# Performance work log

Measured on AMD Instinct MI355X. Metric: run time of the kernel, lower is better.

## Reference

```python
import jax, jax.numpy as jnp
import numpy as np
from jax import lax

V, E, H, B, LP, LQ = 50000, 300, 150, 32, 400, 50


def setup_inputs() -> dict:
    key = jax.random.key(0)
    ks = iter(jax.random.split(key, 40))

    def nrm(shape, s=0.05):
        return jax.random.normal(next(ks), shape, jnp.float32) * s

    emb = nrm((V, E)).at[0].set(0.0)  # padding_idx=0 row is zero
    return dict(
        passage_ids=jax.random.randint(next(ks), (LP, B), 1, V, jnp.int32),
        question_ids=jax.random.randint(next(ks), (LQ, B), 1, V, jnp.int32),
        passage_lens=jax.random.randint(next(ks), (B,), LP // 2, LP + 1, jnp.int32),
        question_lens=jax.random.randint(next(ks), (B,), LQ // 2, LQ + 1, jnp.int32),
        emb=emb,
        plstm_Wih=nrm((4 * H, E)), plstm_Whh=nrm((4 * H, H)), plstm_b=nrm((4 * H,)),
        Wq=nrm((H, H)), Wp=nrm((H, H)), bp=nrm((H,)), Wr=nrm((H, H)),
        wa=nrm((H,)), ba=nrm(()),
        mf_Wih=nrm((4 * H, 2 * H)), mf_Whh=nrm((4 * H, H)), mf_b=nrm((4 * H,)),
        mb_Wih=nrm((4 * H, 2 * H)), mb_Whh=nrm((4 * H, H)), mb_b=nrm((4 * H,)),
        Vm=nrm((H, 2 * H)), Wa_ans=nrm((H, H)), ba_ans=nrm((H,)),
        wb=nrm((H,)), bb=nrm(()),
        ap_Wih=nrm((4 * H, 2 * H)), ap_Whh=nrm((4 * H, H)), ap_b=nrm((4 * H,)),
    )


def _cell(x, h, c, Wih, Whh, b):
    # torch LSTMCell: gate order i, f, g, o; b = b_ih + b_hh
    g = x @ Wih.T + h @ Whh.T + b
    i, f, gg, o = jnp.split(g, 4, axis=-1)
    c2 = jax.nn.sigmoid(f) * c + jax.nn.sigmoid(i) * jnp.tanh(gg)
    return jax.nn.sigmoid(o) * jnp.tanh(c2), c2


def _run_lstm(x, Wih, Whh, b):
    z = jnp.zeros((x.shape[1], Whh.shape[1]), x.dtype)

    def step(carry, xt):
        h, c = carry
        h2, c2 = _cell(xt, h, c, Wih, Whh, b)
        return (h2, c2), h2

    return lax.scan(step, (z, z), x)[1]


def reference(passage_ids, question_ids, passage_lens, question_lens, emb,
              plstm_Wih, plstm_Whh, plstm_b, Wq, Wp, bp, Wr, wa, ba,
              mf_Wih, mf_Whh, mf_b, mb_Wih, mb_Whh, mb_b,
              Vm, Wa_ans, ba_ans, wb, bb, ap_Wih, ap_Whh, ap_b):
    p_mask = (jnp.arange(LP)[:, None] < passage_lens[None, :]).astype(jnp.float32)  # [LP,B]
    q_mask = (jnp.arange(LQ)[:, None] < question_lens[None, :]).astype(jnp.float32)  # [LQ,B]
    # NB: original code (bug) encodes BOTH passage and question with passage_lstm
    Hp = _run_lstm(emb[passage_ids], plstm_Wih, plstm_Whh, plstm_b) * p_mask[:, :, None]
    Hq = _run_lstm(emb[question_ids], plstm_Wih, plstm_Whh, plstm_b) * q_mask[:, :, None]
    aq = Hq @ Wq.T  # [LQ,B,H]

    def match(Hp_seq, m_seq, Wih, Whh, b):
        z0 = jnp.zeros((B, H), jnp.float32)

        def step(carry, inputs):
            h, c = carry
            hp_t, m_t = inputs  # [B,H], [B]
            g = jnp.tanh(aq + (hp_t @ Wp.T + bp)[None] + (h @ Wr.T)[None])  # [LQ,B,H]
            alpha = jax.nn.softmax(g @ wa + ba, axis=0)  # softmax over question positions, [LQ,B]
            wq_t = jnp.einsum('lb,lbh->bh', alpha, Hq)
            zt = jnp.concatenate([hp_t, wq_t], axis=-1) * m_t[:, None]
            h2, c2 = _cell(zt, h, c, Wih, Whh, b)
            h2 = h2 * m_t[:, None]
            c2 = c2 * m_t[:, None]
            return (h2, c2), h2

        return lax.scan(step, (z0, z0), (Hp_seq, m_seq))[1]

    Hf = match(Hp, p_mask, mf_Wih, mf_Whh, mf_b)                    # [LP,B,H]
    Hb = match(Hp[::-1], p_mask[::-1], mb_Wih, mb_Whh, mb_b)[::-1]  # [LP,B,H]
    Hr = jnp.concatenate([Hf, Hb], axis=-1)  # [LP,B,2H]
    am = Hr @ Vm.T  # [LP,B,H]

    ha = jnp.zeros((B, H), jnp.float32)
    ca = jnp.zeros((B, H), jnp.float32)
    dists = []
    for _ in range(2):  # answer-pointer: start / end
        Fk = jnp.tanh(am + (ha @ Wa_ans.T + ba_ans)[None])
        beta = jax.nn.softmax(Fk @ wb + bb, axis=0)  # [LP,B]
        dists.append(beta)
        wHr = jnp.einsum('lb,lbh->bh', beta, Hr)
        ha, ca = _cell(wHr, ha, ca, ap_Wih, ap_Whh, ap_b)
    return jnp.stack(dists)  # [2, LP, B]
```

## Files before the change

### kernel.cpp

```cpp
#include <hip/hip_runtime.h>


typedef _Float16 f16;
typedef f16 f16x2 __attribute__((ext_vector_type(2)));
typedef unsigned int u32;
typedef unsigned short u16;

constexpr int cLP = 400, cLQ = 50, cB = 32, cH = 150, cG = 600;

__device__ __forceinline__ float exp2_(float x){
#if __has_builtin(__builtin_amdgcn_exp2f)
  return __builtin_amdgcn_exp2f(x);
#else
  return exp2f(x);
#endif
}
__device__ __forceinline__ float rcp_(float x){
#if __has_builtin(__builtin_amdgcn_rcpf)
  return __builtin_amdgcn_rcpf(x);
#else
  return 1.0f / x;
#endif
}
__device__ __forceinline__ float sigm(float x){ return rcp_(1.f + exp2_(-1.44269504f * x)); }
__device__ __forceinline__ float tanh_(float x){ return 1.f - 2.f * rcp_(1.f + exp2_(2.88539008f * x)); }

union U2 { u32 u; f16x2 h; };

__device__ __forceinline__ float fdot2_(u32 a, u32 b, float c){
  U2 ua, ub; ua.u = a; ub.u = b;
#if __has_builtin(__builtin_amdgcn_fdot2)
  return __builtin_amdgcn_fdot2(ua.h, ub.h, c, false);
#else
  return c + (float)ua.h[0] * (float)ub.h[0] + (float)ua.h[1] * (float)ub.h[1];
#endif
}
__device__ __forceinline__ u32 pack2(float x, float y){
  U2 p; p.h[0] = (f16)x; p.h[1] = (f16)y; return p.u;
}
__device__ __forceinline__ float2 unp2(u32 v){
  U2 p; p.u = v; return make_float2((float)p.h[0], (float)p.h[1]);
}

__device__ __forceinline__ uint4 ldw4(const float* __restrict__ wr, int i){
  uint4 r;
  r.x = pack2(wr[8*i+0], wr[8*i+1]);
  r.y = pack2(wr[8*i+2], wr[8*i+3]);
  r.z = pack2(wr[8*i+4], wr[8*i+5]);
  r.w = pack2(wr[8*i+6], wr[8*i+7]);
  return r;
}

#define PIN4(v) asm volatile("" : "+v"(v.x), "+v"(v.y), "+v"(v.z), "+v"(v.w));
#define PIN4W(i) PIN4(w##i)
#define PIN4Q(i) PIN4(q##i)

#define REP10(M) M(0) M(1) M(2) M(3) M(4) M(5) M(6) M(7) M(8) M(9)
#define REP6(M) M(0) M(1) M(2) M(3) M(4) M(5)

__global__ __launch_bounds__(256)
void gemm_k(const float* __restrict__ A, const int* __restrict__ ids,
            const float* __restrict__ emb,
            const float* __restrict__ W, int ldw, const float* __restrict__ bias,
            float* __restrict__ Cf, f16* __restrict__ Ch,
            int M, int N, int K)
{
  __shared__ __align__(16) float As[16][68];
  __shared__ __align__(16) float Wt[16][68];
  __shared__ int sids[64];
  int tid = threadIdx.x;
  int n0 = blockIdx.x * 64;
  int m0 = blockIdx.y * 64;
  int tx = tid & 15, ty = tid >> 4;
  if (ids){ if (tid < 64) sids[tid] = ids[m0 + tid]; }
  __syncthreads();

  float acc[4][4] = {};
  int sm = tid >> 2;
  int kq = (tid & 3) << 2;
  const float* arow = ids ? (emb + (size_t)sids[sm] * K)
                          : (A   + (size_t)(m0 + sm) * K);
  const float* wrow = W + (size_t)(n0 + sm) * ldw;
  bool nok = (n0 + sm) < N;

  for (int k0 = 0; k0 < K; k0 += 16){
    #pragma unroll
    for (int p = 0; p < 4; p++){
      int kk = kq + p, k = k0 + kk;
      As[kk][sm] = (k < K) ? arow[k] : 0.f;
      Wt[kk][sm] = (nok && k < K) ? wrow[k] : 0.f;
    }
    __syncthreads();
    #pragma unroll
    for (int kk = 0; kk < 16; kk++){
      float4 av = *(const float4*)&As[kk][ty << 2];
      float4 wv = *(const float4*)&Wt[kk][tx << 2];
      float a[4] = {av.x, av.y, av.z, av.w};
      float w[4] = {wv.x, wv.y, wv.z, wv.w};
      #pragma unroll
      for (int i = 0; i < 4; i++)
        #pragma unroll
        for (int j = 0; j < 4; j++)
          acc[i][j] += a[i] * w[j];
    }
    __syncthreads();
  }
  float bj[4];
  #pragma unroll
  for (int j = 0; j < 4; j++){
    int n = n0 + (tx << 2) + j;
    bj[j] = (bias && n < N) ? bias[n] : 0.f;
  }
  #pragma unroll
  for (int i = 0; i < 4; i++){
    int m = m0 + (ty << 2) + i;
    #pragma unroll
    for (int j = 0; j < 4; j++){
      int n = n0 + (tx << 2) + j;
      if (n < N){
        size_t ci = (size_t)m * N + n;
        float v = acc[i][j] + bj[j];
        if (Ch) Ch[ci] = (f16)v; else Cf[ci] = v;
      }
    }
  }
}

__attribute__((amdgpu_waves_per_eu(1, 3)))
__global__ __launch_bounds__(640)
void enc_k(const float* __restrict__ XGp, const float* __restrict__ XGq,
           const float* __restrict__ Whh,
           const int* __restrict__ plens, const int* __restrict__ qlens,
           float* __restrict__ Hp, float* __restrict__ Hq)
{
  int wg = blockIdx.x;
  bool isq = wg >= cB;
  int b = wg & (cB - 1);
  const float* XG = isq ? XGq : XGp;
  float* Hout = isq ? Hq : Hp;
  int T   = isq ? cLQ : cLP;
  int len = (isq ? qlens : plens)[b];
  int tid = threadIdx.x;

  __shared__ __align__(16) u32 WhhL4[9 * 600 * 4];
  __shared__ float c[cH], gl[cG];
  __shared__ __align__(16) u32 h2s[80];

#define DECLW(i) uint4 w##i;
  REP10(DECLW)
#undef DECLW
  {
    const float* wr = Whh + (size_t)(tid < cG ? tid : 0) * cH;
#define LOADW(i) w##i = ldw4(wr, i);
    REP10(LOADW)
#undef LOADW
    REP10(PIN4W)
  }
  for (int idx = tid; idx < 9 * 600; idx += 640){
    int p4 = idx / 600, r = idx % 600;
    const float* wrow = Whh + (size_t)r * cH + 80;
    uint4 v;
    if (p4 < 8) v = ldw4(wrow, p4);
    else {
      v.x = pack2(wrow[64], wrow[65]);
      v.y = pack2(wrow[66], wrow[67]);
      v.z = pack2(wrow[68], wrow[69]);
      v.w = 0;
    }
    *(uint4*)&WhhL4[idx * 4] = v;
  }
  if (tid < cH) c[tid] = 0.f;
  if (tid < 80) h2s[tid] = 0;
  __syncthreads();

  float xgCur = 0.f;
  if (tid < cG) xgCur = XG[(size_t)b * cG + tid];

  for (int t = 0; t < T; t++){
    int tn = (t + 1 < T) ? t + 1 : t;
    float xgN = 0.f;
    if (tid < cG) xgN = XG[((size_t)tn * cB + b) * cG + tid];

    if (tid < cG){
      float aA = 0.f, aB = 0.f, aC = 0.f, aD = 0.f;
#define DOTW(i) { uint4 hq = *(const uint4*)&h2s[4*(i)]; \
      aA = fdot2_(hq.x, w##i.x, aA); aB = fdot2_(hq.y, w##i.y, aB); \
      aC = fdot2_(hq.z, w##i.z, aC); aD = fdot2_(hq.w, w##i.w, aD); }
      REP10(DOTW)
#undef DOTW
      #pragma unroll
      for (int p4 = 0; p4 < 9; p4++){
        uint4 hq = *(const uint4*)&h2s[40 + 4 * p4];
        uint4 wv = *(const uint4*)&WhhL4[(p4 * 600 + tid) * 4];
        aA = fdot2_(hq.x, wv.x, aA);
        aB = fdot2_(hq.y, wv.y, aB);
        aC = fdot2_(hq.z, wv.z, aC);
        aD = fdot2_(hq.w, wv.w, aD);
      }
      gl[tid] = xgCur + ((aA + aB) + (aC + aD));
    }
    __syncthreads();
    if (tid < 75){
      float hv[2];
      #pragma unroll
      for (int z = 0; z < 2; z++){
        int u = 2 * tid + z;
        float ig = sigm(gl[u]);
        float fg = sigm(gl[cH + u]);
        float gg = tanh_(gl[2 * cH + u]);
        float og = sigm(gl[3 * cH + u]);
        float c2 = fg * c[u] + ig * gg;
        float hh = og * tanh_(c2);
        c[u] = c2;
        hv[z] = hh;
      }
      h2s[tid] = pack2(hv[0], hv[1]);
      float mk = (t < len) ? 1.f : 0.f;
      float2 st; st.x = hv[0] * mk; st.y = hv[1] * mk;
      *(float2*)&Hout[((size_t)t * cB + b) * cH + 2 * tid] = st;
    }
    __syncthreads();
    xgCur = xgN;
  }
}

__attribute__((amdgpu_waves_per_eu(1, 3)))
__global__ __launch_bounds__(640)
void match_k(const f16* __restrict__ XAf, const f16* __restrict__ XAb,
             const f16* __restrict__ QWf, const f16* __restrict__ QWb,
             const float* __restrict__ aq, const float* __restrict__ pp,
             const float* __restrict__ mfWhh, const float* __restrict__ mbWhh,
             const float* __restrict__ mfb, const float* __restrict__ mbb,
             const float* __restrict__ Wr, const float* __restrict__ wa,
             const int* __restrict__ plens, float* __restrict__ Hr)
{
  constexpr int NPAD = 160;
  int wg = blockIdx.x;
  int dir = wg >> 5;
  int b = wg & 31;
  const f16* XA = dir ? XAb : XAf;
  const f16* QW = dir ? QWb : QWf;
  const float* Whh = dir ? mbWhh : mfWhh;
  const float* bm  = dir ? mbb   : mfb;
  int len = plens[b];
  int tid = threadIdx.x;

  __shared__ __align__(16) u32 WhhL4[9 * 600 * 4];
  __shared__ __align__(16) u32 WrT4[20 * 150 * 4];
  __shared__ __align__(16) u32 aq3[cLQ * 96];
  __shared__ float gl[cG];
  __shared__ __align__(16) float sc[NPAD];
  __shared__ __align__(16) float waS[NPAD];
  __shared__ float c[cH];
  __shared__ __align__(16) f16 hsf[160];
  __shared__ float loge[64];
  __shared__ __align__(16) u32 alpha2[28];

#define DECLW(i) uint4 w##i;
  REP10(DECLW)
#undef DECLW
  float bk = 0.f;
  {
    const float* wr = Whh + (size_t)(tid < cG ? tid : 0) * cH;
#define LOADW(i) w##i = ldw4(wr, i);
    REP10(LOADW)
#undef LOADW
    REP10(PIN4W)
    if (tid < cG) bk = bm[tid];
  }
#define DECLQ(i) uint4 q##i;
  REP6(DECLQ)
#undef DECLQ
  u32 q24s;
  {
    const u16* QWu = (const u16*)QW;
    int row = (tid < cG) ? tid : 0;
#define QP(p) ((u32)QWu[((size_t)(2*(p)) * cB + b) * cG + row] | \
               ((u32)QWu[((size_t)(2*(p)+1) * cB + b) * cG + row] << 16))
#define LOADQ(i) q##i.x = QP(4*(i)+0); q##i.y = QP(4*(i)+1); \
                 q##i.z = QP(4*(i)+2); q##i.w = QP(4*(i)+3);
    LOADQ(0) LOADQ(1) LOADQ(2) LOADQ(3) LOADQ(4) LOADQ(5)
    q24s = QP(24);
#undef LOADQ
#undef QP
    REP6(PIN4Q)
    asm volatile("" : "+v"(q24s));
  }
  for (int idx = tid; idx < 9 * 600; idx += 640){
    int p4 = idx / 600, r = idx % 600;
    const float* wrow = Whh + (size_t)r * cH + 80;
    uint4 v;
    if (p4 < 8) v = ldw4(wrow, p4);
    else {
      v.x = pack2(wrow[64], wrow[65]);
      v.y = pack2(wrow[66], wrow[67]);
      v.z = pack2(wrow[68], wrow[69]);
      v.w = 0;
    }
    *(uint4*)&WhhL4[idx * 4] = v;
  }
  for (int idx = tid; idx < 20 * 150; idx += 640){
    int i = idx / 150, j = idx % 150;
    const float* wrow = Wr + (size_t)j * cH;
    uint4 v = {0, 0, 0, 0};
    if (i < 18) v = ldw4(wrow, i);
    else if (i == 18){
      v.x = pack2(wrow[144], wrow[145]);
      v.y = pack2(wrow[146], wrow[147]);
      v.z = pack2(wrow[148], wrow[149]);
      v.w = 0;
    }
    *(uint4*)&WrT4[idx * 4] = v;
  }
  for (int idx = tid; idx < cLQ * 96; idx += 640){
    int l = idx / 96, s = idx % 96;
    int ch = s / 12, t = s % 12;
    u32 v = 0;
    if (t < 10){
      int p = ch * 10 + t;
      if (p < 75){
        const float* ap = aq + ((size_t)l * cB + b) * cH;
        v = pack2(ap[2 * p], ap[2 * p + 1]);
      }
    }
    aq3[idx] = v;
  }
  for (int i = tid; i < NPAD; i += 640) waS[i] = (i < cH) ? wa[i] : 0.f;
  if (tid < cH) c[tid] = 0.f;
  if (tid < 160) hsf[tid] = (f16)0.f;
  if (tid >= cH && tid < NPAD) sc[tid] = 0.f;
  if (tid >= 25 && tid < 28) alpha2[tid] = 0;
  __syncthreads();

  f16 xaCurH = (f16)0.f, xaNxtH = (f16)0.f;
  float ppCur = 0.f, ppNxt = 0.f;
  {
    int t0 = dir ? (cLP - 1) : 0;
    if (tid < cG) xaCurH = XA[((size_t)t0 * cB + b) * cG + tid];
    if (tid < cG && (tid & 3) == 0)
      ppCur = pp[((size_t)t0 * cB + b) * cH + (tid >> 2)];
  }

  for (int s = 0; s < cLP; s++){
    int tt = dir ? (cLP - 1 - s) : s;
    float mk = (tt < len) ? 1.f : 0.f;

    {
      int sn = (s + 1 < cLP) ? s + 1 : s;
      int tn = dir ? (cLP - 1 - sn) : sn;
      if (tid < cG) xaNxtH = XA[((size_t)tn * cB + b) * cG + tid];
      if (tid < cG && (tid & 3) == 0)
        ppNxt = pp[((size_t)tn * cB + b) * cH + (tid >> 2)];
    }

    if (tid < cG){
      int q = tid & 3, j = tid >> 2;
      float sA = 0.f, sB = 0.f, sC = 0.f, sD = 0.f;
      #pragma unroll
      for (int i0 = 0; i0 < 5; i0++){
        int i = 5 * q + i0;
        uint4 hq = *(const uint4*)&hsf[8 * i];
        uint4 wv = *(const uint4*)&WrT4[(i * 150 + j) * 4];
        sA = fdot2_(hq.x, wv.x, sA);
        sB = fdot2_(hq.y, wv.y, sB);
        sC = fdot2_(hq.z, wv.z, sC);
        sD = fdot2_(hq.w, wv.w, sD);
      }
      float v = (sA + sB) + (sC + sD);
      v += __shfl_xor(v, 1);
      v += __shfl_xor(v, 2);
      if (q == 0) sc[j] = v + ppCur;
    }
    __syncthreads();

    if (tid < cG){
      float aA = 0.f, aB = 0.f, aC = 0.f, aD = 0.f;
#define DOTW(i) { uint4 hq = *(const uint4*)&hsf[8*(i)]; \
      aA = fdot2_(hq.x, w##i.x, aA); aB = fdot2_(hq.y, w##i.y, aB); \
      aC = fdot2_(hq.z, w##i.z, aC); aD = fdot2_(hq.w, w##i.w, aD); }
      REP10(DOTW)
#undef DOTW
      #pragma unroll
      for (int p4 = 0; p4 < 9; p4++){
        uint4 hq = *(const uint4*)&hsf[80 + 8 * p4];
        uint4 wv = *(const uint4*)&WhhL4[(p4 * 600 + tid) * 4];
        aA = fdot2_(hq.x, wv.x, aA);
        aB = fdot2_(hq.y, wv.y, aB);
        aC = fdot2_(hq.z, wv.z, aC);
        aD = fdot2_(hq.w, wv.w, aD);
      }
      gl[tid] = bk + ((aA + aB) + (aC + aD));
    }
    if (tid < 400){
      int l = tid >> 3, q8 = tid & 7;
      const u32* ab = aq3 + l * 96 + q8 * 12;
      uint4 A0 = *(const uint4*)(ab);
      uint4 A1 = *(const uint4*)(ab + 4);
      uint2 A2 = *(const uint2*)(ab + 8);
      u32 aqp[10] = {A0.x, A0.y, A0.z, A0.w, A1.x, A1.y, A1.z, A1.w, A2.x, A2.y};
      const float4* scv = (const float4*)(sc  + 20 * q8);
      const float4* wav = (const float4*)(waS + 20 * q8);
      float p0 = 0.f, p1 = 0.f;
      #pragma unroll
      for (int i = 0; i < 5; i++){
        float4 sv = scv[i];
        float4 wv = wav[i];
        float2 a0 = unp2(aqp[2 * i]);
        float2 a1 = unp2(aqp[2 * i + 1]);
        p0 += wv.x * rcp_(1.f + exp2_(2.88539008f * (a0.x + sv.x)));
        p1 += wv.y * rcp_(1.f + exp2_(2.88539008f * (a0.y + sv.y)));
        p0 += wv.z * rcp_(1.f + exp2_(2.88539008f * (a1.x + sv.z)));
        p1 += wv.w * rcp_(1.f + exp2_(2.88539008f * (a1.y + sv.w)));
      }
      float part = p0 + p1;
      part += __shfl_xor(part, 1);
      part += __shfl_xor(part, 2);
      part += __shfl_xor(part, 4);
      if (q8 == 0) loge[l] = part;
    }
    __syncthreads();

    if (tid < 64){
      float lg = (tid < cLQ) ? (-2.f * loge[tid]) : -1e30f;
      float mx = lg;
      #pragma unroll
      for (int off = 32; off; off >>= 1) mx = fmaxf(mx, __shfl_xor(mx, off));
      float e = (tid < cLQ) ? exp2_((lg - mx) * 1.44269504f) : 0.f;
      float sum = e;
      #pragma unroll
      for (int off = 32; off; off >>= 1) sum += __shfl_xor(sum, off);
      float al = e * rcp_(sum);
      float alhi = __shfl_down(al, 1);
      if (tid < cLQ && !(tid & 1)) alpha2[tid >> 1] = pack2(al, alhi);
    }
    __syncthreads();

    if (tid < cG){
      float qA = 0.f, qB = 0.f;
#define DOTQ(i) { uint4 a4 = *(const uint4*)&alpha2[4*(i)]; \
      qA = fdot2_(a4.x, q##i.x, qA); qB = fdot2_(a4.y, q##i.y, qB); \
      qA = fdot2_(a4.z, q##i.z, qA); qB = fdot2_(a4.w, q##i.w, qB); }
      REP6(DOTQ)
#undef DOTQ
      qA = fdot2_(alpha2[24], q24s, qA);
      gl[tid] = gl[tid] + mk * ((float)xaCurH + (qA + qB));
    }
    __syncthreads();

    if (tid < cH){
      float ig = sigm(gl[tid]);
      float fg = sigm(gl[cH + tid]);
      float gg = tanh_(gl[2 * cH + tid]);
      float og = sigm(gl[3 * cH + tid]);
      float c2 = (fg * c[tid] + ig * gg) * mk;
      float hh = og * tanh_(c2) * mk;
      c[tid] = c2;
      hsf[tid] = (f16)hh;
      Hr[((size_t)tt * cB + b) * (2 * cH) + dir * cH + tid] = hh;
    }
    __syncthreads();

    xaCurH = xaNxtH;
    ppCur  = ppNxt;
  }
}

__global__ __launch_bounds__(640)
void ptr_k(const float* __restrict__ am, const float* __restrict__ Hr,
           const float* __restrict__ Wa, const float* __restrict__ baa,
           const float* __restrict__ wb,
           const float* __restrict__ apWih, const float* __restrict__ apWhh,
             const float* __restrict__ apb, float* __restrict__ out)
{
  int b = blockIdx.x, tid = threadIdx.x;
  __shared__ float ha[cH], ca[cH], haWa[160], wbs[160];
  __shared__ float beta[cLP], wHr[2 * cH], gl[cG], red[20];
  if (tid < cH){ ha[tid] = 0.f; ca[tid] = 0.f; }
  if (tid < 160) wbs[tid] = (tid < cH) ? wb[tid] : 0.f;
  __syncthreads();

  for (int it = 0; it < 2; ++it){
    if (tid < cH){
      float acc = baa[tid];
      const float* wr = Wa + (size_t)tid * cH;
      for (int i = 0; i < cH; i++) acc += ha[i] * wr[i];
      haWa[tid] = acc;
    } else if (tid < 160) haWa[tid] = 0.f;
    __syncthreads();

    {
      int tt = tid >> 4;
      int jq = tid & 15;
      for (int t0 = 0; t0 < cLP; t0 += 40){
        int t = t0 + tt;
        float part = 0.f;
        const float* amr = am + ((size_t)t * cB + b) * cH;
        #pragma unroll
        for (int i = 0; i < 10; i++){
          int j = jq * 10 + i;
          if (j < cH){
            float F = tanh_(amr[j] + haWa[j]);
            part += wbs[j] * F;
          }
        }
        part += __shfl_xor(part, 1);
        part += __shfl_xor(part, 2);
        part += __shfl_xor(part, 4);
        part += __shfl_xor(part, 8);
        if (jq == 0) beta[t] = part;
      }
    }
    __syncthreads();

    float x = (tid < cLP) ? beta[tid] : -1e30f;
    float mx = x;
    #pragma unroll
    for (int off = 32; off; off >>= 1) mx = fmaxf(mx, __shfl_xor(mx, off));
    if ((tid & 63) == 0) red[tid >> 6] = mx;
    __syncthreads();
    if (tid == 0){
      float m2 = red[0];
      for (int w = 1; w < 10; w++) m2 = fmaxf(m2, red[w]);
      red[16] = m2;
    }
    __syncthreads();
    mx = red[16];
    float e = (tid < cLP) ? exp2_((x - mx) * 1.44269504f) : 0.f;
    float sm = e;
    #pragma unroll
    for (int off = 32; off; off >>= 1) sm += __shfl_xor(sm, off);
    if ((tid & 63) == 0) red[tid >> 6] = sm;
    __syncthreads();
    if (tid == 0){
      float s2 = 0.f;
      for (int w = 0; w < 10; w++) s2 += red[w];
      red[17] = s2;
    }
    __syncthreads();
    float bsum = red[17];
    if (tid < cLP){
      float bt = e * rcp_(bsum);
      beta[tid] = bt;
      out[(size_t)it * cLP * cB + (size_t)tid * cB + b] = bt;
    }
    __syncthreads();

    if (tid < 2 * cH){
      float acc = 0.f;
      for (int t = 0; t < cLP; t++)
        acc += beta[t] * Hr[((size_t)t * cB + b) * (2 * cH) + tid];
      wHr[tid] = acc;
    }
    __syncthreads();

    if (tid < cG){
      float acc = apb[tid];
      const float* r1 = apWih + (size_t)tid * (2 * cH);
      for (int i = 0; i < 2 * cH; i++) acc += wHr[i] * r1[i];
      const float* r2 = apWhh + (size_t)tid * cH;
      for (int i = 0; i < cH; i++) acc += ha[i] * r2[i];
      gl[tid] = acc;
    }
    __syncthreads();
    if (tid < cH){
      float ig = sigm(gl[tid]);
      float fg = sigm(gl[cH + tid]);
      float gg = tanh_(gl[2 * cH + tid]);
      float og = sigm(gl[3 * cH + tid]);
      float c2 = fg * ca[tid] + ig * gg;
      ca[tid] = c2;
      ha[tid] = og * tanh_(c2);
    }
    __syncthreads();
  }
}

extern "C" void kernel_launch(void* const* d_in, const int* in_sizes, int n_in,
                              void* d_out, int out_size, void* d_ws, size_t ws_size,
                              hipStream_t stream)
{
  (void)in_sizes; (void)n_in; (void)out_size; (void)ws_size;
  const int*   p_ids = (const int*)d_in[0];
  const int*   q_ids = (const int*)d_in[1];
  const int*   plens = (const int*)d_in[2];
  const int*   qlens = (const int*)d_in[3];
  const float* emb   = (const float*)d_in[4];
  const float* pWih  = (const float*)d_in[5];
  const float* pWhh  = (const float*)d_in[6];
  const float* pb    = (const float*)d_in[7];
  const float* Wq    = (const float*)d_in[8];
  const float* Wp    = (const float*)d_in[9];
  const float* bp    = (const float*)d_in[10];
  const float* Wr    = (const float*)d_in[11];
  const float* wa    = (const float*)d_in[12];
  const float* mfWih = (const float*)d_in[14];
  const float* mfWhh = (const float*)d_in[15];
  const float* mfb   = (const float*)d_in[16];
  const float* mbWih = (const float*)d_in[17];
  const float* mbWhh = (const float*)d_in[18];
  const float* mbb   = (const float*)d_in[19];
  const float* Vm    = (const float*)d_in[20];
  const float* Waa   = (const float*)d_in[21];
  const float* baa   = (const float*)d_in[22];
  const float* wb    = (const float*)d_in[23];
  const float* apWih = (const float*)d_in[25];
  const float* apWhh = (const float*)d_in[26];
  const float* apb   = (const float*)d_in[27];
  float* out = (float*)d_out;

  float* ws  = (float*)d_ws;
  float* XGp = ws;
  float* XGq = ws + 7680000;
  f16*   XAb = (f16*)(ws + 8640000);
  float* Hp  = ws + 12480000;
  float* Hq  = ws + 14400000;
  float* aqb = ws + 14640000;
  float* ppb = ws + 14880000;
  float* Hr  = ws + 16800000;
  float* am  = ws + 20640000;
  f16*   XAf = (f16*)XGp;
  f16*   QWf = (f16*)XGq;
  f16*   QWb = QWf + (size_t)1600 * 600;

  dim3 blk(256);
  gemm_k<<<dim3(10,200), blk, 0, stream>>>(nullptr, p_ids, emb, pWih, 300, pb,
                                           XGp, nullptr, 12800, 600, 300);
  gemm_k<<<dim3(10, 25), blk, 0, stream>>>(nullptr, q_ids, emb, pWih, 300, pb,
                                           XGq, nullptr, 1600, 600, 300);
  enc_k<<<64, 640, 0, stream>>>(XGp, XGq, pWhh, plens, qlens, Hp, Hq);
  gemm_k<<<dim3(3,200), blk, 0, stream>>>(Hp, nullptr, nullptr, Wp, 150, bp,
                                          ppb, nullptr, 12800, 150, 150);
  gemm_k<<<dim3(3, 25), blk, 0, stream>>>(Hq, nullptr, nullptr, Wq, 150, nullptr,
                                          aqb, nullptr, 1600, 150, 150);
  gemm_k<<<dim3(10,200), blk, 0, stream>>>(Hp, nullptr, nullptr, mfWih, 300, nullptr,
                                           nullptr, XAf, 12800, 600, 150);
  gemm_k<<<dim3(10,200), blk, 0, stream>>>(Hp, nullptr, nullptr, mbWih, 300, nullptr,
                                           nullptr, XAb, 12800, 600, 150);
  gemm_k<<<dim3(10, 25), blk, 0, stream>>>(Hq, nullptr, nullptr, mfWih + 150, 300, nullptr,
                                           nullptr, QWf, 1600, 600, 150);
  gemm_k<<<dim3(10, 25), blk, 0, stream>>>(Hq, nullptr, nullptr, mbWih + 150, 300, nullptr,
                                           nullptr, QWb, 1600, 600, 150);
  match_k<<<64, 640, 0, stream>>>(XAf, XAb, QWf, QWb, aqb, ppb, mfWhh, mbWhh,
                                  mfb, mbb, Wr, wa, plens, Hr);
  gemm_k<<<dim3(3,200), blk, 0, stream>>>(Hr, nullptr, nullptr, Vm, 300, nullptr,
                                          am, nullptr, 12800, 150, 300);
  ptr_k<<<32, 640, 0, stream>>>(am, Hr, Waa, baa, wb, apWih, apWhh, apb, out);
}
```

Baseline: 2.238 ms.

## Remap gate rows so LSTM cell update uses wave shuffles, removing barriers

Threads are remapped so each 64-lane wave holds all four gates (i,f,g,o) for 16 hidden units, with the gate index in bits 4-5 of the lane id. Gate nonlinearities are then computed in parallel per lane and combined through cross-lane shuffles, which removes the gl shared buffer and one barrier per timestep in both the encoder and match kernels. In the match kernel the Wr score dot product is also merged into the same phase as the Whh dot, dropping another barrier. The cost is 640 threads with some idle lanes (u>=150) and a wider f16 hidden buffer in the encoder.

Result: slower. 4.071 ms (+81.9%).

```diff
diff --git a/kernel.cpp b/kernel.cpp
--- a/kernel.cpp
+++ b/kernel.cpp
@@ -141,24 +141,28 @@
   int T   = isq ? cLQ : cLP;
   int len = (isq ? qlens : plens)[b];
   int tid = threadIdx.x;
+  int u = (tid & 15) + ((tid >> 6) << 4);
+  int q = (tid >> 4) & 3;
+  int r = q * cH + u;
+  bool act = (u < cH);
 
   __shared__ __align__(16) u32 WhhL4[9 * 600 * 4];
-  __shared__ float c[cH], gl[cG];
-  __shared__ __align__(16) u32 h2s[80];
+  __shared__ float c[cH];
+  __shared__ __align__(16) f16 hsf[160];
 
 #define DECLW(i) uint4 w##i;
   REP10(DECLW)
 #undef DECLW
   {
-    const float* wr = Whh + (size_t)(tid < cG ? tid : 0) * cH;
+    const float* wr = Whh + (size_t)(act ? r : 0) * cH;
 #define LOADW(i) w##i = ldw4(wr, i);
     REP10(LOADW)
 #undef LOADW
     REP10(PIN4W)
   }
   for (int idx = tid; idx < 9 * 600; idx += 640){
-    int p4 = idx / 600, r = idx % 600;
-    const float* wrow = Whh + (size_t)r * cH + 80;
+    int p4 = idx / 600, rr = idx % 600;
+    const float* wrow = Whh + (size_t)rr * cH + 80;
     uint4 v;
     if (p4 < 8) v = ldw4(wrow, p4);
     else {
@@ -170,54 +174,46 @@
     *(uint4*)&WhhL4[idx * 4] = v;
   }
   if (tid < cH) c[tid] = 0.f;
-  if (tid < 80) h2s[tid] = 0;
+  if (tid < 160) hsf[tid] = (f16)0.f;
   __syncthreads();
 
   float xgCur = 0.f;
-  if (tid < cG) xgCur = XG[(size_t)b * cG + tid];
+  if (act) xgCur = XG[(size_t)b * cG + r];
 
   for (int t = 0; t < T; t++){
     int tn = (t + 1 < T) ? t + 1 : t;
     float xgN = 0.f;
-    if (tid < cG) xgN = XG[((size_t)tn * cB + b) * cG + tid];
-
-    if (tid < cG){
+    if (act) xgN = XG[((size_t)tn * cB + b) * cG + r];
+
+    if (act){
       float aA = 0.f, aB = 0.f, aC = 0.f, aD = 0.f;
-#define DOTW(i) { uint4 hq = *(const uint4*)&h2s[4*(i)]; \
+#define DOTW(i) { uint4 hq = *(const uint4*)&hsf[8*(i)]; \
       aA = fdot2_(hq.x, w##i.x, aA); aB = fdot2_(hq.y, w##i.y, aB); \
       aC = fdot2_(hq.z, w##i.z, aC); aD = fdot2_(hq.w, w##i.w, aD); }
       REP10(DOTW)
 #undef DOTW
       #pragma unroll
       for (int p4 = 0; p4 < 9; p4++){
-        uint4 hq = *(const uint4*)&h2s[40 + 4 * p4];
-        uint4 wv = *(const uint4*)&WhhL4[(p4 * 600 + tid) * 4];
+        uint4 hq = *(const uint4*)&hsf[80 + 8 * p4];
+        uint4 wv = *(const uint4*)&WhhL4[(p4 * 600 + r) * 4];
         aA = fdot2_(hq.x, wv.x, aA);
         aB = fdot2_(hq.y, wv.y, aB);
         aC = fdot2_(hq.z, wv.z, aC);
         aD = fdot2_(hq.w, wv.w, aD);
       }
-      gl[tid] = xgCur + ((aA + aB) + (aC + aD));
-    }
-    __syncthreads();
-    if (tid < 75){
-      float hv[2];
-      #pragma unroll
-      for (int z = 0; z < 2; z++){
-        int u = 2 * tid + z;
-        float ig = sigm(gl[u]);
-        float fg = sigm(gl[cH + u]);
-        float gg = tanh_(gl[2 * cH + u]);
-        float og = sigm(gl[3 * cH + u]);
-        float c2 = fg * c[u] + ig * gg;
-        float hh = og * tanh_(c2);
+      float gv = xgCur + ((aA + aB) + (aC + aD));
+      float tv = (q == 2) ? tanh_(gv) : sigm(gv);
+      float tB = __shfl_xor(tv, 16);
+      float tC = __shfl_xor(tv, 32);
+      float tD = __shfl_xor(tB, 32);
+      if (q == 0){
+        float c2 = tB * c[u] + tv * tC;
+        float hh = tD * tanh_(c2);
         c[u] = c2;
-        hv[z] = hh;
-      }
-      h2s[tid] = pack2(hv[0], hv[1]);
-      float mk = (t < len) ? 1.f : 0.f;
-      float2 st; st.x = hv[0] * mk; st.y = hv[1] * mk;
-      *(float2*)&Hout[((size_t)t * cB + b) * cH + 2 * tid] = st;
+        hsf[u] = (f16)hh;
+        float mk = (t < len) ? 1.f : 0.f;
+        Hout[((size_t)t * cB + b) * cH + u] = hh * mk;
+      }
     }
     __syncthreads();
     xgCur = xgN;
@@ -244,11 +240,14 @@
   const float* bm  = dir ? mbb   : mfb;
   int len = plens[b];
   int tid = threadIdx.x;
+  int u = (tid & 15) + ((tid >> 6) << 4);
+  int q = (tid >> 4) & 3;
+  int r = q * cH + u;
+  bool act = (u < cH);
 
   __shared__ __align__(16) u32 WhhL4[9 * 600 * 4];
   __shared__ __align__(16) u32 WrT4[20 * 150 * 4];
   __shared__ __align__(16) u32 aq3[cLQ * 96];
-  __shared__ float gl[cG];
   __shared__ __align__(16) float sc[NPAD];
   __shared__ __align__(16) float waS[NPAD];
   __shared__ float c[cH];
@@ -261,12 +260,12 @@
 #undef DECLW
   float bk = 0.f;
   {
-    const float* wr = Whh + (size_t)(tid < cG ? tid : 0) * cH;
+    const float* wr = Whh + (size_t)(act ? r : 0) * cH;
 #define LOADW(i) w##i = ldw4(wr, i);
     REP10(LOADW)
 #undef LOADW
     REP10(PIN4W)
-    if (tid < cG) bk = bm[tid];
+    if (act) bk = bm[r];
   }
 #define DECLQ(i) uint4 q##i;
   REP6(DECLQ)
@@ -274,7 +273,7 @@
   u32 q24s;
   {
     const u16* QWu = (const u16*)QW;
-    int row = (tid < cG) ? tid : 0;
+    int row = act ? r : 0;
 #define QP(p) ((u32)QWu[((size_t)(2*(p)) * cB + b) * cG + row] | \
                ((u32)QWu[((size_t)(2*(p)+1) * cB + b) * cG + row] << 16))
 #define LOADQ(i) q##i.x = QP(4*(i)+0); q##i.y = QP(4*(i)+1); \
@@ -287,8 +286,8 @@
     asm volatile("" : "+v"(q24s));
   }
   for (int idx = tid; idx < 9 * 600; idx += 640){
-    int p4 = idx / 600, r = idx % 600;
-    const float* wrow = Whh + (size_t)r * cH + 80;
+    int p4 = idx / 600, rr = idx % 600;
+    const float* wrow = Whh + (size_t)rr * cH + 80;
     uint4 v;
     if (p4 < 8) v = ldw4(wrow, p4);
     else {
@@ -336,9 +335,8 @@
   float ppCur = 0.f, ppNxt = 0.f;
   {
     int t0 = dir ? (cLP - 1) : 0;
-    if (tid < cG) xaCurH = XA[((size_t)t0 * cB + b) * cG + tid];
-    if (tid < cG && (tid & 3) == 0)
-      ppCur = pp[((size_t)t0 * cB + b) * cH + (tid >> 2)];
+    if (act) xaCurH = XA[((size_t)t0 * cB + b) * cG + r];
+    if (act && q == 0) ppCur = pp[((size_t)t0 * cB + b) * cH + u];
   }
 
   for (int s = 0; s < cLP; s++){
@@ -348,32 +346,12 @@
     {
       int sn = (s + 1 < cLP) ? s + 1 : s;
       int tn = dir ? (cLP - 1 - sn) : sn;
-      if (tid < cG) xaNxtH = XA[((size_t)tn * cB + b) * cG + tid];
-      if (tid < cG && (tid & 3) == 0)
-        ppNxt = pp[((size_t)tn * cB + b) * cH + (tid >> 2)];
-    }
-
-    if (tid < cG){
-      int q = tid & 3, j = tid >> 2;
-      float sA = 0.f, sB = 0.f, sC = 0.f, sD = 0.f;
-      #pragma unroll
-      for (int i0 = 0; i0 < 5; i0++){
-        int i = 5 * q + i0;
-        uint4 hq = *(const uint4*)&hsf[8 * i];
-        uint4 wv = *(const uint4*)&WrT4[(i * 150 + j) * 4];
-        sA = fdot2_(hq.x, wv.x, sA);
-        sB = fdot2_(hq.y, wv.y, sB);
-        sC = fdot2_(hq.z, wv.z, sC);
-        sD = fdot2_(hq.w, wv.w, sD);
-      }
-      float v = (sA + sB) + (sC + sD);
-      v += __shfl_xor(v, 1);
-      v += __shfl_xor(v, 2);
-      if (q == 0) sc[j] = v + ppCur;
-    }
-    __syncthreads();
-
-    if (tid < cG){
+      if (act) xaNxtH = XA[((size_t)tn * cB + b) * cG + r];
+      if (act && q == 0) ppNxt = pp[((size_t)tn * cB + b) * cH + u];
+    }
+
+    float gpre = 0.f;
+    if (act){
       float aA = 0.f, aB = 0.f, aC = 0.f, aD = 0.f;
 #define DOTW(i) { uint4 hq = *(const uint4*)&hsf[8*(i)]; \
       aA = fdot2_(hq.x, w##i.x, aA); aB = fdot2_(hq.y, w##i.y, aB); \
@@ -383,14 +361,32 @@
       #pragma unroll
       for (int p4 = 0; p4 < 9; p4++){
         uint4 hq = *(const uint4*)&hsf[80 + 8 * p4];
-        uint4 wv = *(const uint4*)&WhhL4[(p4 * 600 + tid) * 4];
+        uint4 wv = *(const uint4*)&WhhL4[(p4 * 600 + r) * 4];
         aA = fdot2_(hq.x, wv.x, aA);
         aB = fdot2_(hq.y, wv.y, aB);
         aC = fdot2_(hq.z, wv.z, aC);
         aD = fdot2_(hq.w, wv.w, aD);
       }
-      gl[tid] = bk + ((aA + aB) + (aC + aD));
-    }
+      gpre = bk + ((aA + aB) + (aC + aD));
+
+      float sA = 0.f, sB = 0.f, sC = 0.f, sD = 0.f;
+      #pragma unroll
+      for (int i0 = 0; i0 < 5; i0++){
+        int i = 5 * q + i0;
+        uint4 hq = *(const uint4*)&hsf[8 * i];
+        uint4 wv = *(const uint4*)&WrT4[(i * 150 + u) * 4];
+        sA = fdot2_(hq.x, wv.x, sA);
+        sB = fdot2_(hq.y, wv.y, sB);
+        sC = fdot2_(hq.z, wv.z, sC);
+        sD = fdot2_(hq.w, wv.w, sD);
+      }
+      float v = (sA + sB) + (sC + sD);
+      v += __shfl_xor(v, 16);
+      v += __shfl_xor(v, 32);
+      if (q == 0) sc[u] = v + ppCur;
+    }
+    __syncthreads();
+
     if (tid < 400){
       int l = tid >> 3, q8 = tid & 7;
       const u32* ab = aq3 + l * 96 + q8 * 12;
@@ -435,7 +431,7 @@
     }
     __syncthreads();
 
-    if (tid < cG){
+    if (act){
       float qA = 0.f, qB = 0.f;
 #define DOTQ(i) { uint4 a4 = *(const uint4*)&alpha2[4*(i)]; \
       qA = fdot2_(a4.x, q##i.x, qA); qB = fdot2_(a4.y, q##i.y, qB); \
@@ -443,20 +439,18 @@
       REP6(DOTQ)
 #undef DOTQ
       qA = fdot2_(alpha2[24], q24s, qA);
-      gl[tid] = gl[tid] + mk * ((float)xaCurH + (qA + qB));
-    }
-    __syncthreads();
-
-    if (tid < cH){
-      float ig = sigm(gl[tid]);
-      float fg = sigm(gl[cH + tid]);
-      float gg = tanh_(gl[2 * cH + tid]);
-      float og = sigm(gl[3 * cH + tid]);
-      float c2 = (fg * c[tid] + ig * gg) * mk;
-      float hh = og * tanh_(c2) * mk;
-      c[tid] = c2;
-      hsf[tid] = (f16)hh;
-      Hr[((size_t)tt * cB + b) * (2 * cH) + dir * cH + tid] = hh;
+      float gv = gpre + mk * ((float)xaCurH + (qA + qB));
+      float tv = (q == 2) ? tanh_(gv) : sigm(gv);
+      float tB = __shfl_xor(tv, 16);
+      float tC = __shfl_xor(tv, 32);
+      float tD = __shfl_xor(tB, 32);
+      if (q == 0){
+        float c2 = (tB * c[u] + tv * tC) * mk;
+        float hh = tD * tanh_(c2) * mk;
+        c[u] = c2;
+        hsf[u] = (f16)hh;
+        Hr[((size_t)tt * cB + b) * (2 * cH) + dir * cH + u] = hh;
+      }
     }
     __syncthreads();
 
```
